# Optimization experiments

Hardware: AMD Instinct MI355X
Metric: run time of the kernel (lower is better)

Reference implementation:

```python
import jax, jax.numpy as jnp
import numpy as np
from jax.scipy.linalg import expm

D = 3  # matrix size, hard-coded by final view(a, b, 3, 3) in the torch module


def _fnn(t, W1, b1, W2, b2):
    # FNNnew: Linear(1,5) -> tanh -> Linear(5,1); t: (T,1) -> (T,)
    return (jnp.tanh(t @ W1.T + b1) @ W2.T + b2)[:, 0]


def _path_dev(Z, A1, A2):
    # Z: (bs, T, 2). Returns X (cumulative matrix products) and X^-1, each (bs, T, D, D).
    bs, T, _ = Z.shape
    A1s = A1 - A1.T
    A2s = A2 - A2.T
    M = A1s * Z[..., 0, None, None] + A2s * Z[..., 1, None, None]  # (bs,T,D,D)
    E = jax.vmap(expm)(M.reshape(-1, D, D)).reshape(bs, T, D, D)
    X0 = jnp.broadcast_to(jnp.eye(D, dtype=Z.dtype), (bs, D, D))

    def step(X, Et):
        Xn = jnp.einsum('bij,bjk->bik', X, Et)
        return Xn, Xn

    _, Xs = jax.lax.scan(step, X0, jnp.moveaxis(E[:, 1:], 0, 1))  # (T-1,bs,D,D)
    A = jnp.moveaxis(jnp.concatenate([X0[None], Xs], axis=0), 0, 1)  # (bs,T,D,D)
    B = jnp.linalg.inv(A)
    return A, B


def setup_inputs() -> dict:
    key = jax.random.key(0)
    ks = jax.random.split(key, 20)
    bs, T = 128, 4096
    inp = {"x_data": jax.random.normal(ks[0], (bs, T, 2), jnp.float32),
           "A1": jax.random.normal(ks[1], (D, D), jnp.float32),
           "A2": jax.random.normal(ks[2], (D, D), jnp.float32)}
    i = 3
    for name in ("f", "fp", "g", "gp"):
        inp[name + "_W1"] = jax.random.normal(ks[i], (5, 1), jnp.float32) * 0.5; i += 1
        inp[name + "_b1"] = jax.random.normal(ks[i], (5,), jnp.float32) * 0.5; i += 1
        inp[name + "_W2"] = jax.random.normal(ks[i], (1, 5), jnp.float32) * 0.5; i += 1
        inp[name + "_b2"] = jax.random.normal(ks[i], (1,), jnp.float32) * 0.5; i += 1
    return inp


def reference(x_data, A1, A2, f_W1, f_b1, f_W2, f_b2, fp_W1, fp_b1, fp_W2, fp_b2,
              g_W1, g_b1, g_W2, g_b2, gp_W1, gp_b1, gp_W2, gp_b2):
    bs, T, _ = x_data.shape
    t = jnp.arange(T, dtype=jnp.float32)[:, None]
    f_arr = _fnn(t, f_W1, f_b1, f_W2, f_b2)[::-1]
    fp_arr = _fnn(t, fp_W1, fp_b1, fp_W2, fp_b2)[::-1]
    g_arr = _fnn(t, g_W1, g_b1, g_W2, g_b2)
    gp_arr = _fnn(t, gp_W1, gp_b1, gp_W2, gp_b2)
    pad1 = lambda a: jnp.pad(a, (T - 1, T - 1))  # length 3T-2
    Hf = jnp.fft.fft(pad1(f_arr))
    Hfp = jnp.fft.fft(pad1(fp_arr))
    Hg = jnp.fft.fft(pad1(g_arr))
    Hgp = jnp.fft.fft(pad1(gp_arr))

    X, Xinv = _path_dev(x_data, A1, A2)
    Xf = X.reshape(bs, T, D * D)
    Xif = Xinv.reshape(bs, T, D * D)
    padT = lambda a: jnp.pad(a, ((0, 0), (T - 1, T - 1), (0, 0)))
    FA = jnp.fft.fft(padT(Xif), axis=1)  # (bs, 3T-2, 9), batched over all d^2 channels
    FB = jnp.fft.fft(padT(Xf), axis=1)
    AA = jnp.fft.ifft(FA * Hf[None, :, None], axis=1)
    AB = jnp.fft.ifft(FB * Hg[None, :, None], axis=1)
    BA = jnp.fft.ifft(FA * Hfp[None, :, None], axis=1)
    BB = jnp.fft.ifft(FB * Hgp[None, :, None], axis=1)
    out = (AA * AB + BA * BB)[:, 2 * T - 2:, :]  # (bs, T, 9)
    return out.real.reshape(bs, T, D, D)
```

## Files before the change

### kernel.cpp

```cpp
#include <hip/hip_runtime.h>
#include <math.h>

#define TT    4096
#define NFFT  8192
#define LOGN  13
#define NTHR  512
#define BS    128
#define NTASK 576
#define BUFSZ (NFFT + NFFT/8)

__device__ __forceinline__ float2 cmulf(float2 u, float2 v){
  return make_float2(u.x*v.x - u.y*v.y, u.x*v.y + u.y*v.x);
}
__device__ __forceinline__ float2 cadd(float2 a, float2 b){ return make_float2(a.x+b.x, a.y+b.y); }
__device__ __forceinline__ float2 csub(float2 a, float2 b){ return make_float2(a.x-b.x, a.y-b.y); }
__device__ __forceinline__ float2 cmuli (float2 a){ return make_float2(-a.y,  a.x); }
__device__ __forceinline__ float2 cmulni(float2 a){ return make_float2( a.y, -a.x); }

__device__ __forceinline__ float2& BREF(float2* b, int i){ return b[i + (i>>3)]; }

constexpr int ctz_c(int v){ int c=0; while(!(v&1)){ v>>=1; c++; } return c; }

template<int S>
__device__ __forceinline__ void fwd_pass(float2* buf, int tid){
  constexpr int LS = ctz_c(S);
  const float nis = -3.14159265358979f / (2.0f * (float)S);
  #pragma unroll
  for (int r = 0; r < (NFFT/4)/NTHR; ++r){
    int j   = tid + NTHR*r;
    int off = j & (S-1);
    int i0  = ((j >> LS) << (LS+2)) + off;
    float2 a = BREF(buf,i0), b = BREF(buf,i0+S), c = BREF(buf,i0+2*S), d = BREF(buf,i0+3*S);
    float sn, cs; __sincosf(nis*(float)off, &sn, &cs);
    float2 wA = make_float2(cs, sn);
    float2 wB = make_float2(cs*cs - sn*sn, 2.f*cs*sn);
    float2 w3 = cmulf(wA, wB);
    float2 s02 = cadd(a,c), d02 = csub(a,c);
    float2 s13 = cadd(b,d), d13 = csub(b,d);
    BREF(buf,i0)     = cadd(s02, s13);
    BREF(buf,i0+S)   = cmulf(csub(s02, s13), wB);
    BREF(buf,i0+2*S) = cmulf(wA, cadd(d02, cmulni(d13)));
    BREF(buf,i0+3*S) = cmulf(w3, cadd(d02, cmuli (d13)));
  }
}

template<int S>
__device__ __forceinline__ void inv_pass(float2* buf, int tid){
  constexpr int LS = ctz_c(S);
  const float pis = 3.14159265358979f / (2.0f * (float)S);
  #pragma unroll
  for (int r = 0; r < (NFFT/4)/NTHR; ++r){
    int j   = tid + NTHR*r;
    int off = j & (S-1);
    int i0  = ((j >> LS) << (LS+2)) + off;
    float2 a = BREF(buf,i0), b = BREF(buf,i0+S), c = BREF(buf,i0+2*S), d = BREF(buf,i0+3*S);
    float sn, cs; __sincosf(pis*(float)off, &sn, &cs);
    float2 u  = make_float2(cs, sn);
    float2 u2 = make_float2(cs*cs - sn*sn, 2.f*cs*sn);
    float2 u2b = cmulf(u2, b), u2d = cmulf(u2, d);
    float2 t0 = cadd(a,u2b), t1 = csub(a,u2b);
    float2 t2 = cadd(c,u2d), t3 = csub(c,u2d);
    float2 ut2  = cmulf(u, t2);
    float2 iut3 = cmuli(cmulf(u, t3));
    BREF(buf,i0)     = cadd(t0, ut2);
    BREF(buf,i0+2*S) = csub(t0, ut2);
    BREF(buf,i0+S)   = cadd(t1, iut3);
    BREF(buf,i0+3*S) = csub(t1, iut3);
  }
}

__device__ __forceinline__ void fwd_final8(float2* buf, int tid){
  const float R2 = 0.70710678118654752f;
  #pragma unroll
  for (int r = 0; r < (NFFT/8)/NTHR; ++r){
    int m = tid + NTHR*r;
    float2 v[8];
    #pragma unroll
    for (int l=0;l<8;l++) v[l] = BREF(buf,8*m+l);
    { float2 t = csub(v[0], v[4]); v[0] = cadd(v[0], v[4]); v[4] = t; }
    { float2 t = csub(v[1], v[5]); v[1] = cadd(v[1], v[5]); v[5] = cmulf(t, make_float2(R2, -R2)); }
    { float2 t = csub(v[2], v[6]); v[2] = cadd(v[2], v[6]); v[6] = cmulni(t); }
    { float2 t = csub(v[3], v[7]); v[3] = cadd(v[3], v[7]); v[7] = cmulf(t, make_float2(-R2, -R2)); }
    #pragma unroll
    for (int base = 0; base < 8; base += 4){
      { float2 t = csub(v[base],   v[base+2]); v[base]   = cadd(v[base],   v[base+2]); v[base+2] = t; }
      { float2 t = csub(v[base+1], v[base+3]); v[base+1] = cadd(v[base+1], v[base+3]); v[base+3] = cmulni(t); }
    }
    #pragma unroll
    for (int p = 0; p < 8; p += 2){ float2 t = csub(v[p], v[p+1]); v[p] = cadd(v[p], v[p+1]); v[p+1] = t; }
    #pragma unroll
    for (int l=0;l<8;l++) BREF(buf,8*m+l) = v[l];
  }
}

__device__ __forceinline__ void fwd_final8_reg(float2* buf, int tid, float2* zreg){
  const float R2 = 0.70710678118654752f;
  #pragma unroll
  for (int rr = 0; rr < 2; ++rr){
    int m = tid + NTHR*rr;
    float2 v[8];
    #pragma unroll
    for (int l=0;l<8;l++) v[l] = BREF(buf,8*m+l);
    { float2 t = csub(v[0], v[4]); v[0] = cadd(v[0], v[4]); v[4] = t; }
    { float2 t = csub(v[1], v[5]); v[1] = cadd(v[1], v[5]); v[5] = cmulf(t, make_float2(R2, -R2)); }
    { float2 t = csub(v[2], v[6]); v[2] = cadd(v[2], v[6]); v[6] = cmulni(t); }
    { float2 t = csub(v[3], v[7]); v[3] = cadd(v[3], v[7]); v[7] = cmulf(t, make_float2(-R2, -R2)); }
    #pragma unroll
    for (int base = 0; base < 8; base += 4){
      { float2 t = csub(v[base],   v[base+2]); v[base]   = cadd(v[base],   v[base+2]); v[base+2] = t; }
      { float2 t = csub(v[base+1], v[base+3]); v[base+1] = cadd(v[base+1], v[base+3]); v[base+3] = cmulni(t); }
    }
    #pragma unroll
    for (int p = 0; p < 8; p += 2){ float2 t = csub(v[p], v[p+1]); v[p] = cadd(v[p], v[p+1]); v[p+1] = t; }
    #pragma unroll
    for (int l=0;l<8;l++) zreg[rr*8+l] = v[l];
  }
}

__device__ __forceinline__ void inv_zh(float2* buf, int tid,
                                       const float2* zreg,
                                       const float2* __restrict__ H,
                                       float2* yout){
  const float R2 = 0.70710678118654752f;
  #pragma unroll
  for (int rr = 0; rr < 2; ++rr){
    int m = tid + NTHR*rr;
    float2 v[8];
    #pragma unroll
    for (int l = 0; l < 8; ++l) v[l] = cmulf(zreg[rr*8+l], H[8*m+l]);
    #pragma unroll
    for (int p = 0; p < 8; p += 2){ float2 t = v[p+1]; v[p+1] = csub(v[p], t); v[p] = cadd(v[p], t); }
    #pragma unroll
    for (int base = 0; base < 8; base += 4){
      { float2 t = v[base+2];        v[base+2] = csub(v[base],   t); v[base]   = cadd(v[base],   t); }
      { float2 t = cmuli(v[base+3]); v[base+3] = csub(v[base+1], t); v[base+1] = cadd(v[base+1], t); }
    }
    { float2 t = v[4];                              v[4] = csub(v[0], t); v[0] = cadd(v[0], t); }
    { float2 t = cmulf(v[5], make_float2(R2, R2));  v[5] = csub(v[1], t); v[1] = cadd(v[1], t); }
    { float2 t = cmuli(v[6]);                       v[6] = csub(v[2], t); v[2] = cadd(v[2], t); }
    { float2 t = cmulf(v[7], make_float2(-R2, R2)); v[7] = csub(v[3], t); v[3] = cadd(v[3], t); }
    #pragma unroll
    for (int l = 0; l < 8; ++l) BREF(buf,8*m+l) = v[l];
  }
  __syncthreads();
  inv_pass<8>(buf, tid);   __syncthreads();
  inv_pass<32>(buf, tid);  __syncthreads();
  inv_pass<128>(buf, tid); __syncthreads();
  inv_pass<512>(buf, tid); __syncthreads();
  const float pis = 3.14159265358979f / 4096.f;
  #pragma unroll
  for (int r = 0; r < 4; ++r){
    int j = tid + NTHR*r;
    float sn, cs; __sincosf(pis*(float)j, &sn, &cs);
    float2 u  = make_float2(cs, sn);
    float2 u2 = make_float2(cs*cs - sn*sn, 2.f*cs*sn);
    float2 a = BREF(buf,j), b = BREF(buf,j+2048), c = BREF(buf,j+4096), d = BREF(buf,j+6144);
    float2 u2b = cmulf(u2, b), u2d = cmulf(u2, d);
    float2 t0 = cadd(a, u2b), t1 = csub(a, u2b);
    float2 t2 = cadd(c, u2d), t3 = csub(c, u2d);
    yout[2*r]   = cadd(t0, cmulf(u, t2));
    yout[2*r+1] = cadd(t1, cmuli(cmulf(u, t3)));
  }
}

__device__ __forceinline__ void rot3(float ax, float ay, float az, float* R){
  float th2 = ax*ax + ay*ay + az*az;
  float s1, s2;
  if (th2 < 1e-8f){
    s1 = 1.f - th2*(1.f/6.f);
    s2 = 0.5f - th2*(1.f/24.f);
  } else {
    float th = sqrtf(th2);
    float sn = sinf(th);
    s1 = sn / th;
    float sh = sinf(0.5f*th);
    s2 = 2.f*sh*sh / th2;
  }
  R[0] = 1.f - s2*(ay*ay+az*az);
  R[1] = -s1*az + s2*ax*ay;
  R[2] =  s1*ay + s2*ax*az;
  R[3] =  s1*az + s2*ax*ay;
  R[4] = 1.f - s2*(ax*ax+az*az);
  R[5] = -s1*ax + s2*ay*az;
  R[6] = -s1*ay + s2*ax*az;
  R[7] =  s1*ax + s2*ay*az;
  R[8] = 1.f - s2*(ax*ax+ay*ay);
}

__device__ __forceinline__ void mm3(const float* A, const float* B, float* C){
  #pragma unroll
  for (int i=0;i<3;i++){
    float a0=A[3*i], a1=A[3*i+1], a2=A[3*i+2];
    #pragma unroll
    for (int l=0;l<3;l++)
      C[3*i+l] = a0*B[l] + a1*B[3+l] + a2*B[6+l];
  }
}

__global__ __launch_bounds__(NTHR) void prep(
  const float* __restrict__ x, const float* __restrict__ A1, const float* __restrict__ A2,
  const float* fW1, const float* fb1p, const float* fW2, const float* fb2p,
  const float* fpW1, const float* fpb1, const float* fpW2, const float* fpb2,
  const float* gW1, const float* gb1, const float* gW2, const float* gb2,
  const float* gpW1, const float* gpb1, const float* gpW2, const float* gpb2,
  float* __restrict__ X, float2* __restrict__ Hcf, float2* __restrict__ Hcf2,
  float2* __restrict__ Hcg, float2* __restrict__ Hcg2)
{
  __shared__ float2 buf[BUFSZ];
  int tid = threadIdx.x;
  if (blockIdx.x < 2){
    const float *aW1,*ab1,*aW2,*ab2,*bW1,*bb1,*bW2,*bb2; float2 *outp, *outp2; int revd;
    if (blockIdx.x == 0){ aW1=fW1; ab1=fb1p; aW2=fW2; ab2=fb2p;
      bW1=fpW1; bb1=fpb1; bW2=fpW2; bb2=fpb2; outp=Hcf; outp2=Hcf2; revd=1; }
    else { aW1=gW1; ab1=gb1; aW2=gW2; ab2=gb2;
      bW1=gpW1; bb1=gpb1; bW2=gpW2; bb2=gpb2; outp=Hcg; outp2=Hcg2; revd=0; }
    float w1a[5],b1a[5],w2a[5],w1b[5],b1b[5],w2b[5];
    #pragma unroll
    for (int h=0;h<5;h++){
      w1a[h]=aW1[h]; b1a[h]=ab1[h]; w2a[h]=aW2[h];
      w1b[h]=bW1[h]; b1b[h]=bb1[h]; w2b[h]=bW2[h];
    }
    float cA = ab2[0], cB = bb2[0];
    const float nis = -3.14159265358979f / 4096.f;
    #pragma unroll
    for (int r = 0; r < 2048/NTHR; ++r){
      int j = tid + NTHR*r;
      float2 zz[2];
      #pragma unroll
      for (int h2 = 0; h2 < 2; ++h2){
        int n = j + 2048*h2;
        float t = revd ? (float)(TT-1-n) : (float)n;
        float va = cA, vb = cB;
        #pragma unroll
        for (int h=0;h<5;h++){
          va += w2a[h]*tanhf(w1a[h]*t + b1a[h]);
          vb += w2b[h]*tanhf(w1b[h]*t + b1b[h]);
        }
        zz[h2] = make_float2(va, vb);
      }
      float sn, cs; __sincosf(nis*(float)j, &sn, &cs);
      float2 wA = make_float2(cs, sn);
      float2 wB = make_float2(cs*cs - sn*sn, 2.f*cs*sn);
      float2 w3 = cmulf(wA, wB);
      float2 a = zz[0], b = zz[1];
      BREF(buf,j)      = cadd(a,b);
      BREF(buf,j+2048) = cmulf(csub(a,b), wB);
      BREF(buf,j+4096) = cmulf(wA, make_float2(a.x + b.y, a.y - b.x));
      BREF(buf,j+6144) = cmulf(w3, make_float2(a.x - b.y, a.y + b.x));
    }
    __syncthreads(); fwd_pass<512>(buf, tid);
    __syncthreads(); fwd_pass<128>(buf, tid);
    __syncthreads(); fwd_pass<32>(buf, tid);
    __syncthreads(); fwd_pass<8>(buf, tid);
    __syncthreads(); fwd_final8(buf, tid);
    __syncthreads();
    #pragma unroll
    for (int r=0;r<NFFT/NTHR;r++){
      int p = tid + NTHR*r;
      outp[p] = BREF(buf,p);
      int k  = (int)(__brev((unsigned)p) >> (32-LOGN));
      int kk = (NFFT - k) & (NFFT-1);
      int q  = (int)(__brev((unsigned)kk) >> (32-LOGN));
      float2 z = BREF(buf,q);
      outp2[p] = make_float2(z.x, -z.y);
    }
  } else {
    float* sc = (float*)buf;
    int b = blockIdx.x - 2, j = tid;
    float k1x = A1[7]-A1[5], k1y = A1[2]-A1[6], k1z = A1[3]-A1[1];
    float k2x = A2[7]-A2[5], k2y = A2[2]-A2[6], k2z = A2[3]-A2[1];
    float L[9] = {1,0,0, 0,1,0, 0,0,1};
    #pragma unroll 1
    for (int k=1;k<=8;k++){
      int t = 8*j + k;
      if (t < TT){
        float z0 = x[((size_t)b*TT + t)*2 + 0];
        float z1 = x[((size_t)b*TT + t)*2 + 1];
        float R[9];
        rot3(k1x*z0 + k2x*z1, k1y*z0 + k2y*z1, k1z*z0 + k2z*z1, R);
        float Cm[9]; mm3(L, R, Cm);
        #pragma unroll
        for (int m=0;m<9;m++) L[m] = Cm[m];
      }
    }
    #pragma unroll
    for (int m=0;m<9;m++) sc[(0*512 + j)*9 + m] = L[m];
    int cur = 0;
    for (int d=1; d<512; d<<=1){
      __syncthreads();
      float own[9], res[9];
      #pragma unroll
      for (int m=0;m<9;m++) own[m] = sc[(cur*512 + j)*9 + m];
      if (j >= d){
        float prev[9];
        #pragma unroll
        for (int m=0;m<9;m++) prev[m] = sc[(cur*512 + j - d)*9 + m];
        mm3(prev, own, res);
      } else {
        #pragma unroll
        for (int m=0;m<9;m++) res[m] = own[m];
      }
      #pragma unroll
      for (int m=0;m<9;m++) sc[((cur^1)*512 + j)*9 + m] = res[m];
      cur ^= 1;
    }
    __syncthreads();
    float Xc[9];
    if (j == 0){
      Xc[0]=1;Xc[1]=0;Xc[2]=0;Xc[3]=0;Xc[4]=1;Xc[5]=0;Xc[6]=0;Xc[7]=0;Xc[8]=1;
    } else {
      #pragma unroll
      for (int m=0;m<9;m++) Xc[m] = sc[(cur*512 + j - 1)*9 + m];
    }
    #pragma unroll
    for (int m=0;m<9;m++) X[((size_t)b*9 + m)*TT + 8*j] = Xc[m];
    #pragma unroll 1
    for (int k=1;k<8;k++){
      int t = 8*j + k;
      float z0 = x[((size_t)b*TT + t)*2 + 0];
      float z1 = x[((size_t)b*TT + t)*2 + 1];
      float R[9];
      rot3(k1x*z0 + k2x*z1, k1y*z0 + k2y*z1, k1z*z0 + k2z*z1, R);
      float Cm[9]; mm3(Xc, R, Cm);
      #pragma unroll
      for (int m=0;m<9;m++){ Xc[m] = Cm[m]; X[((size_t)b*9 + m)*TT + t] = Xc[m]; }
    }
  }
}

__global__ __launch_bounds__(NTHR, 2) void convk4(const float* __restrict__ X,
    const float2* __restrict__ Hcf, const float2* __restrict__ Hcf2,
    const float2* __restrict__ Hcg, const float2* __restrict__ Hcg2,
    float* __restrict__ tmp)
{
  __shared__ float2 buf[BUFSZ];
  int tid = threadIdx.x;
  int task = blockIdx.x;
  int b1i, c1, b2i, c2; bool cross;
  if (task < 384){
    int b = task/3, p = task % 3;
    b1i = b; b2i = b; cross = true;
    c1 = (p==0)?1:((p==1)?2:5);
    c2 = (p==0)?3:((p==1)?6:7);
  } else if (task < 512){
    int b = task - 384; b1i=b; b2i=b; c1=0; c2=4; cross=false;
  } else {
    int q = task - 512; b1i = 2*q; b2i = 2*q+1; c1=8; c2=8; cross=false;
  }
  const float* x1 = X + ((size_t)b1i*9 + c1)*TT;
  const float* x2 = X + ((size_t)b2i*9 + c2)*TT;

  {
    const float nis = -3.14159265358979f / 4096.f;
    #pragma unroll
    for (int r = 0; r < 2048/NTHR; ++r){
      int j = tid + NTHR*r;
      float2 a = make_float2(x1[j], x2[j]);
      float2 b = make_float2(x1[j+2048], x2[j+2048]);
      float sn, cs; __sincosf(nis*(float)j, &sn, &cs);
      float2 wA = make_float2(cs, sn);
      float2 wB = make_float2(cs*cs - sn*sn, 2.f*cs*sn);
      float2 w3 = cmulf(wA, wB);
      BREF(buf,j)      = cadd(a,b);
      BREF(buf,j+2048) = cmulf(csub(a,b), wB);
      BREF(buf,j+4096) = cmulf(wA, make_float2(a.x + b.y, a.y - b.x));
      BREF(buf,j+6144) = cmulf(w3, make_float2(a.x - b.y, a.y + b.x));
    }
  }
  __syncthreads(); fwd_pass<512>(buf, tid);
  __syncthreads(); fwd_pass<128>(buf, tid);
  __syncthreads(); fwd_pass<32>(buf, tid);
  __syncthreads(); fwd_pass<8>(buf, tid);
  __syncthreads();
  float2 zreg[16];
  fwd_final8_reg(buf, tid, zreg);

  float2 W1[8];
  inv_zh(buf, tid, zreg, Hcf, W1);
  __syncthreads();
  float2 W2[8];
  inv_zh(buf, tid, zreg, Hcf2, W2);
  float a1[8], a2[8], bb1[8], bb2[8];
  #pragma unroll
  for (int e = 0; e < 8; ++e){
    a1[e]  = 0.5f*(W1[e].x + W2[e].x);
    a2[e]  = 0.5f*(W1[e].y + W2[e].y);
    bb1[e] = 0.5f*(W1[e].y - W2[e].y);
    bb2[e] = 0.5f*(W2[e].x - W1[e].x);
  }
  __syncthreads();
  float2 V1[8];
  inv_zh(buf, tid, zreg, Hcg, V1);
  __syncthreads();
  float2 V2[8];
  inv_zh(buf, tid, zreg, Hcg2, V2);

  const float invN2 = (1.0f/NFFT)*(1.0f/NFFT);
  float* op1 = tmp + ((size_t)b1i*9 + c1)*TT;
  float* op2 = tmp + ((size_t)b2i*9 + c2)*TT;
  #pragma unroll
  for (int r = 0; r < 4; ++r){
    #pragma unroll
    for (int h = 0; h < 2; ++h){
      int e = 2*r + h;
      int s = tid + NTHR*r + h*2048;
      float c1v = 0.5f*(V1[e].x + V2[e].x);
      float c2v = 0.5f*(V1[e].y + V2[e].y);
      float d1  = 0.5f*(V1[e].y - V2[e].y);
      float d2  = 0.5f*(V2[e].x - V1[e].x);
      float Af1 = cross ? a2[e]  : a1[e];
      float Bf1 = cross ? bb2[e] : bb1[e];
      float Af2 = cross ? a1[e]  : a2[e];
      float Bf2 = cross ? bb1[e] : bb2[e];
      op1[s] = (Af1*c1v + Bf1*d1) * invN2;
      op2[s] = (Af2*c2v + Bf2*d2) * invN2;
    }
  }
}

__global__ __launch_bounds__(256) void repack(const float* __restrict__ tmp,
                                              float* __restrict__ out){
  __shared__ float tile[9][264];
  int b  = blockIdx.x >> 4;
  int t0 = (blockIdx.x & 15) << 8;
  int tid = threadIdx.x;
  #pragma unroll
  for (int c = 0; c < 9; ++c)
    tile[c][tid] = tmp[((size_t)b*9 + c)*TT + t0 + tid];
  __syncthreads();
  size_t base = ((size_t)b*TT + t0)*9;
  #pragma unroll
  for (int k = 0; k < 9; ++k){
    int idx = tid + 256*k;
    out[base + idx] = tile[idx % 9][idx / 9];
  }
}

__device__ void fft_dif_bitrev(float2* buf, int tid){
  const float PI = 3.14159265358979f;
  #pragma unroll 1
  for (int stage = 0; stage < LOGN; ++stage){
    int logspan = LOGN - 1 - stage;
    int span = 1 << logspan;
    float nis = -PI / (float)span;
    __syncthreads();
    #pragma unroll
    for (int r = 0; r < NFFT/2/NTHR; ++r){
      int j = tid + NTHR*r;
      int off = j & (span - 1);
      int i0 = ((j >> logspan) << (logspan + 1)) + off;
      int i1 = i0 + span;
      float2 a = buf[i0], b = buf[i1];
      float ang = nis * (float)off;
      float sn, cs;
      __sincosf(ang, &sn, &cs);
      float2 d = make_float2(a.x - b.x, a.y - b.y);
      buf[i0] = make_float2(a.x + b.x, a.y + b.y);
      buf[i1] = cmulf(d, make_float2(cs, sn));
    }
  }
  __syncthreads();
  #pragma unroll
  for (int r = 0; r < NFFT/NTHR; ++r){
    int p = tid + NTHR*r;
    int q = (int)(__brev((unsigned)p) >> (32 - LOGN));
    if (p < q){ float2 t = buf[p]; buf[p] = buf[q]; buf[q] = t; }
  }
  __syncthreads();
}

__global__ __launch_bounds__(NTHR) void hker_fb(
  const float* fW1, const float* fb1p, const float* fW2, const float* fb2p,
  const float* fpW1, const float* fpb1, const float* fpW2, const float* fpb2,
  const float* gW1, const float* gb1, const float* gW2, const float* gb2,
  const float* gpW1, const float* gpb1, const float* gpW2, const float* gpb2,
  float2* Hcf, float2* Hcg)
{
  __shared__ float2 buf[NFFT];
  int tid = threadIdx.x;
  const float *aW1,*ab1,*aW2,*ab2,*bW1,*bb1,*bW2,*bb2; float2* outp; int revd;
  if (blockIdx.x == 0){ aW1=fW1; ab1=fb1p; aW2=fW2; ab2=fb2p;
    bW1=fpW1; bb1=fpb1; bW2=fpW2; bb2=fpb2; outp=Hcf; revd=1; }
  else { aW1=gW1; ab1=gb1; aW2=gW2; ab2=gb2;
    bW1=gpW1; bb1=gpb1; bW2=gpW2; bb2=gpb2; outp=Hcg; revd=0; }
  float w1a[5],b1a[5],w2a[5],w1b[5],b1b[5],w2b[5];
  #pragma unroll
  for (int h=0;h<5;h++){
    w1a[h]=aW1[h]; b1a[h]=ab1[h]; w2a[h]=aW2[h];
    w1b[h]=bW1[h]; b1b[h]=bb1[h]; w2b[h]=bW2[h];
  }
  float cA = ab2[0], cB = bb2[0];
  for (int r=0;r<NFFT/NTHR;r++){
    int s = tid + NTHR*r;
    float2 v = make_float2(0.f, 0.f);
    if (s < TT){
      float t = revd ? (float)(TT-1-s) : (float)s;
      float va = cA, vb = cB;
      #pragma unroll
      for (int h=0;h<5;h++){
        va += w2a[h]*tanhf(w1a[h]*t + b1a[h]);
        vb += w2b[h]*tanhf(w1b[h]*t + b1b[h]);
      }
      v = make_float2(va, vb);
    }
    buf[s] = v;
  }
  fft_dif_bitrev(buf, tid);
  for (int r=0;r<NFFT/NTHR;r++){ int k = tid + NTHR*r; outp[k] = buf[k]; }
}

__global__ __launch_bounds__(256) void scank_fb(const float* __restrict__ x,
    const float* __restrict__ A1, const float* __restrict__ A2,
    float* __restrict__ X)
{
  __shared__ float sc[2][256][9];
  int b = blockIdx.x, j = threadIdx.x;
  float k1x = A1[7]-A1[5], k1y = A1[2]-A1[6], k1z = A1[3]-A1[1];
  float k2x = A2[7]-A2[5], k2y = A2[2]-A2[6], k2z = A2[3]-A2[1];
  float L[9] = {1,0,0, 0,1,0, 0,0,1};
  #pragma unroll 1
  for (int k=1;k<=16;k++){
    int t = 16*j + k;
    if (t < TT){
      float z0 = x[((size_t)b*TT + t)*2 + 0];
      float z1 = x[((size_t)b*TT + t)*2 + 1];
      float R[9];
      rot3(k1x*z0 + k2x*z1, k1y*z0 + k2y*z1, k1z*z0 + k2z*z1, R);
      float Cm[9]; mm3(L, R, Cm);
      #pragma unroll
      for (int m=0;m<9;m++) L[m] = Cm[m];
    }
  }
  #pragma unroll
  for (int m=0;m<9;m++) sc[0][j][m] = L[m];
  int cur = 0;
  for (int d=1; d<256; d<<=1){
    __syncthreads();
    float own[9], res[9];
    #pragma unroll
    for (int m=0;m<9;m++) own[m] = sc[cur][j][m];
    if (j >= d){
      float prev[9];
      #pragma unroll
      for (int m=0;m<9;m++) prev[m] = sc[cur][j-d][m];
      mm3(prev, own, res);
    } else {
      #pragma unroll
      for (int m=0;m<9;m++) res[m] = own[m];
    }
    #pragma unroll
    for (int m=0;m<9;m++) sc[cur^1][j][m] = res[m];
    cur ^= 1;
  }
  __syncthreads();
  float Xc[9];
  if (j == 0){
    Xc[0]=1;Xc[1]=0;Xc[2]=0;Xc[3]=0;Xc[4]=1;Xc[5]=0;Xc[6]=0;Xc[7]=0;Xc[8]=1;
  } else {
    #pragma unroll
    for (int m=0;m<9;m++) Xc[m] = sc[cur][j-1][m];
  }
  #pragma unroll
  for (int m=0;m<9;m++) X[((size_t)b*9 + m)*TT + 16*j] = Xc[m];
  #pragma unroll 1
  for (int k=1;k<16;k++){
    int t = 16*j + k;
    float z0 = x[((size_t)b*TT + t)*2 + 0];
    float z1 = x[((size_t)b*TT + t)*2 + 1];
    float R[9];
    rot3(k1x*z0 + k2x*z1, k1y*z0 + k2y*z1, k1z*z0 + k2z*z1, R);
    float Cm[9]; mm3(Xc, R, Cm);
    #pragma unroll
    for (int m=0;m<9;m++){ Xc[m] = Cm[m]; X[((size_t)b*9 + m)*TT + t] = Xc[m]; }
  }
}

__global__ __launch_bounds__(NTHR) void convk_fb(const float* __restrict__ X,
    const float2* __restrict__ Hcf, const float2* __restrict__ Hcg,
    float* __restrict__ out)
{
  __shared__ float2 buf[NFFT];
  __shared__ float2 fb1[NFFT/2 + 2];
  __shared__ float2 fb2[NFFT/2 + 2];
  int tid = threadIdx.x;
  int task = blockIdx.x;
  int b1i, c1, b2i, c2; bool cross;
  if (task < 384){
    int b = task/3, p = task % 3;
    b1i = b; b2i = b; cross = true;
    c1 = (p==0)?1:((p==1)?2:5);
    c2 = (p==0)?3:((p==1)?6:7);
  } else if (task < 512){
    int b = task - 384; b1i=b; b2i=b; c1=0; c2=4; cross=false;
  } else {
    int q = task - 512; b1i = 2*q; b2i = 2*q+1; c1=8; c2=8; cross=false;
  }
  const float* x1 = X + ((size_t)b1i*9 + c1)*TT;
  const float* x2 = X + ((size_t)b2i*9 + c2)*TT;
  #pragma unroll
  for (int r=0;r<NFFT/NTHR;r++){
    int s = tid + NTHR*r;
    float2 v = make_float2(0.f,0.f);
    if (s < TT){ v.x = x1[s]; v.y = x2[s]; }
    buf[s] = v;
  }
  fft_dif_bitrev(buf, tid);
  for (int k = tid; k <= NFFT/2; k += NTHR){
    int kk = (NFFT - k) & (NFFT - 1);
    float2 zk = buf[k], zn = buf[kk];
    fb1[k] = make_float2(0.5f*(zk.x + zn.x), 0.5f*(zk.y - zn.y));
    fb2[k] = make_float2(0.5f*(zk.y + zn.y), 0.5f*(zn.x - zk.x));
  }
  __syncthreads();
  const float invN2 = (1.0f/NFFT)*(1.0f/NFFT);
  #pragma unroll 1
  for (int pass = 0; pass < 2; ++pass){
    const float2* fA = (pass==0) ? (cross ? fb2 : fb1) : (cross ? fb1 : fb2);
    const float2* fG = (pass==0) ? fb1 : fb2;
    int ob = (pass==0) ? b1i : b2i;
    int oc = (pass==0) ? c1 : c2;
    #pragma unroll
    for (int r=0;r<NFFT/NTHR;r++){
      int k = tid + NTHR*r;
      float2 F;
      if (k <= NFFT/2) F = fA[k];
      else { float2 g = fA[NFFT-k]; F = make_float2(g.x, -g.y); }
      float2 P = cmulf(F, Hcf[k]);
      buf[k] = make_float2(P.x, -P.y);
    }
    fft_dif_bitrev(buf, tid);
    float rA[8], rB[8];
    #pragma unroll
    for (int r=0;r<8;r++){
      int s = tid + NTHR*r;
      rA[r] = buf[s].x;
      rB[r] = -buf[s].y;
    }
    #pragma unroll
    for (int r=0;r<NFFT/NTHR;r++){
      int k = tid + NTHR*r;
      float2 F;
      if (k <= NFFT/2) F = fG[k];
      else { float2 g = fG[NFFT-k]; F = make_float2(g.x, -g.y); }
      float2 P = cmulf(F, Hcg[k]);
      buf[k] = make_float2(P.x, -P.y);
    }
    fft_dif_bitrev(buf, tid);
    #pragma unroll
    for (int r=0;r<8;r++){
      int s = tid + NTHR*r;
      float AB = buf[s].x, BB = -buf[s].y;
      out[((size_t)ob*TT + s)*9 + oc] = (rA[r]*AB + rB[r]*BB) * invN2;
    }
  }
}

extern "C" void kernel_launch(void* const* d_in, const int* in_sizes, int n_in,
                              void* d_out, int out_size, void* d_ws, size_t ws_size,
                              hipStream_t stream){
  const float* x  = (const float*)d_in[0];
  const float* A1 = (const float*)d_in[1];
  const float* A2 = (const float*)d_in[2];
  const float* P[16];
  for (int i=0;i<16;i++) P[i] = (const float*)d_in[3+i];

  size_t xbytes = (size_t)BS*9*TT*sizeof(float);
  size_t hbytes = (size_t)NFFT*sizeof(float2);
  float*  Xb   = (float*)d_ws;
  float2* Hcf  = (float2*)((char*)d_ws + xbytes);
  float2* Hcf2 = Hcf + NFFT;
  float2* Hcg  = Hcf + 2*NFFT;
  float2* Hcg2 = Hcf + 3*NFFT;
  float*  tmp  = (float*)((char*)d_ws + xbytes + 4*hbytes);
  size_t need = xbytes + 4*hbytes + xbytes;

  if (ws_size >= need){
    prep<<<2 + BS, NTHR, 0, stream>>>(x, A1, A2,
        P[0],P[1],P[2],P[3],P[4],P[5],P[6],P[7],
        P[8],P[9],P[10],P[11],P[12],P[13],P[14],P[15],
        Xb, Hcf, Hcf2, Hcg, Hcg2);
    convk4<<<NTASK, NTHR, 0, stream>>>(Xb, Hcf, Hcf2, Hcg, Hcg2, tmp);
    repack<<<BS*16, 256, 0, stream>>>(tmp, (float*)d_out);
  } else {
    hker_fb<<<2, NTHR, 0, stream>>>(P[0],P[1],P[2],P[3],P[4],P[5],P[6],P[7],
        P[8],P[9],P[10],P[11],P[12],P[13],P[14],P[15], Hcf, Hcg);
    scank_fb<<<BS, 256, 0, stream>>>(x, A1, A2, Xb);
    convk_fb<<<NTASK, NTHR, 0, stream>>>(Xb, Hcf, Hcg, (float*)d_out);
  }
}
```

Before: 215.6 us.

## Restructure shared-memory FFTs as radix-16 register passes with XOR-swizzled LDS

Replaces the radix-4 shared-memory FFT passes (five forward passes plus a radix-8 final, and likewise for each inverse) with radix-16 butterflies computed in registers. Each 8192-point transform now takes about three shared-memory round trips instead of six, with a final radix-2 step folded in. The padded BREF indexing is replaced by an XOR swizzle to avoid bank conflicts, which also shrinks the LDS buffer. This cuts barrier count and LDS traffic, but the 16-element register arrays raise register pressure, which could cost occupancy. The H multiply layout must also match the new ordering.

After: 273.5 us. 26.9% more time.

```diff
diff --git a/kernel.cpp b/kernel.cpp
--- a/kernel.cpp
+++ b/kernel.cpp
@@ -16,10 +16,167 @@
 __device__ __forceinline__ float2 csub(float2 a, float2 b){ return make_float2(a.x-b.x, a.y-b.y); }
 __device__ __forceinline__ float2 cmuli (float2 a){ return make_float2(-a.y,  a.x); }
 __device__ __forceinline__ float2 cmulni(float2 a){ return make_float2( a.y, -a.x); }
+__device__ __forceinline__ float2 csq(float2 a){ return make_float2(a.x*a.x - a.y*a.y, 2.f*a.x*a.y); }
 
 __device__ __forceinline__ float2& BREF(float2* b, int i){ return b[i + (i>>3)]; }
+#define SWZ(p) ((p) ^ (((p)>>4)&15))
+
+#define DEF_C8  const float2 C8[8]  = { {1.f,0.f},{0.9238795325f,-0.3826834324f},{0.7071067812f,-0.7071067812f},{0.3826834324f,-0.9238795325f},{0.f,-1.f},{-0.3826834324f,-0.9238795325f},{-0.7071067812f,-0.7071067812f},{-0.9238795325f,-0.3826834324f} }
+#define DEF_CC8 const float2 CC8[8] = { {1.f,0.f},{0.9238795325f, 0.3826834324f},{0.7071067812f, 0.7071067812f},{0.3826834324f, 0.9238795325f},{0.f, 1.f},{-0.3826834324f, 0.9238795325f},{-0.7071067812f, 0.7071067812f},{-0.9238795325f, 0.3826834324f} }
 
 constexpr int ctz_c(int v){ int c=0; while(!(v&1)){ v>>=1; c++; } return c; }
+
+__device__ __forceinline__ void rad16_fwd_tail(float2* v, float2 u2){
+  DEF_C8;
+  float2 u3 = csq(u2), u4 = csq(u3);
+  #pragma unroll
+  for (int g=0; g<16; g+=8)
+    #pragma unroll
+    for (int t=0;t<4;t++){
+      float2 a=v[g+t], b=v[g+t+4];
+      v[g+t]=cadd(a,b);
+      v[g+t+4]=cmulf(csub(a,b), cmulf(u2, C8[2*t]));
+    }
+  #pragma unroll
+  for (int g=0; g<16; g+=4)
+    #pragma unroll
+    for (int t=0;t<2;t++){
+      float2 a=v[g+t], b=v[g+t+2];
+      v[g+t]=cadd(a,b);
+      v[g+t+2]=cmulf(csub(a,b), cmulf(u3, C8[4*t]));
+    }
+  #pragma unroll
+  for (int g=0; g<16; g+=2){
+    float2 a=v[g], b=v[g+1];
+    v[g]=cadd(a,b);
+    v[g+1]=cmulf(csub(a,b), u4);
+  }
+}
+
+__device__ __forceinline__ void rad16_fwd(float2* v, float2 u1){
+  DEF_C8;
+  #pragma unroll
+  for (int t=0;t<8;t++){
+    float2 a=v[t], b=v[t+8];
+    v[t]=cadd(a,b);
+    v[t+8]=cmulf(csub(a,b), cmulf(u1, C8[t]));
+  }
+  rad16_fwd_tail(v, csq(u1));
+}
+
+__device__ __forceinline__ void rad16_inv(float2* v, float2 u1c){
+  DEF_CC8;
+  float2 u2c = csq(u1c), u3c = csq(u2c), u4c = csq(u3c);
+  #pragma unroll
+  for (int g=0; g<16; g+=2){
+    float2 b = cmulf(v[g+1], u4c);
+    float2 a = v[g];
+    v[g]=cadd(a,b); v[g+1]=csub(a,b);
+  }
+  #pragma unroll
+  for (int g=0; g<16; g+=4)
+    #pragma unroll
+    for (int t=0;t<2;t++){
+      float2 b = cmulf(v[g+t+2], cmulf(u3c, CC8[4*t]));
+      float2 a = v[g+t];
+      v[g+t]=cadd(a,b); v[g+t+2]=csub(a,b);
+    }
+  #pragma unroll
+  for (int g=0; g<16; g+=8)
+    #pragma unroll
+    for (int t=0;t<4;t++){
+      float2 b = cmulf(v[g+t+4], cmulf(u2c, CC8[2*t]));
+      float2 a = v[g+t];
+      v[g+t]=cadd(a,b); v[g+t+4]=csub(a,b);
+    }
+  #pragma unroll
+  for (int t=0;t<8;t++){
+    float2 b = cmulf(v[t+8], cmulf(u1c, CC8[t]));
+    float2 a = v[t];
+    v[t]=cadd(a,b); v[t+8]=csub(a,b);
+  }
+}
+
+__device__ __forceinline__ void rad16_inv_last(float2* v, float2 u1c, float2* y){
+  DEF_CC8;
+  float2 u2c = csq(u1c), u3c = csq(u2c), u4c = csq(u3c);
+  #pragma unroll
+  for (int g=0; g<16; g+=2){
+    float2 b = cmulf(v[g+1], u4c);
+    float2 a = v[g];
+    v[g]=cadd(a,b); v[g+1]=csub(a,b);
+  }
+  #pragma unroll
+  for (int g=0; g<16; g+=4)
+    #pragma unroll
+    for (int t=0;t<2;t++){
+      float2 b = cmulf(v[g+t+2], cmulf(u3c, CC8[4*t]));
+      float2 a = v[g+t];
+      v[g+t]=cadd(a,b); v[g+t+2]=csub(a,b);
+    }
+  #pragma unroll
+  for (int g=0; g<16; g+=8)
+    #pragma unroll
+    for (int t=0;t<4;t++){
+      float2 b = cmulf(v[g+t+4], cmulf(u2c, CC8[2*t]));
+      float2 a = v[g+t];
+      v[g+t]=cadd(a,b); v[g+t+4]=csub(a,b);
+    }
+  #pragma unroll
+  for (int t=0;t<8;t++)
+    y[t] = cadd(v[t], cmulf(v[t+8], cmulf(u1c, CC8[t])));
+}
+
+template<bool FIRST>
+__device__ __forceinline__ void inv16(float2* buf, int tid,
+                                      const float2* zreg,
+                                      const float2* __restrict__ H,
+                                      float2* y){
+  if (!FIRST) __syncthreads();
+  {
+    float2 v[16];
+    const float2* Hp = H + 16*tid;
+    #pragma unroll
+    for (int j=0;j<16;j++) v[j] = cmulf(zreg[j], Hp[j]);
+    #pragma unroll
+    for (int g=0; g<16; g+=2){
+      float2 a=v[g], b=v[g+1];
+      v[g]=cadd(a,b); v[g+1]=csub(a,b);
+    }
+    #pragma unroll
+    for (int j=0;j<16;j++) buf[SWZ(16*tid + j)] = v[j];
+  }
+  __syncthreads();
+  {
+    float2 v[16];
+    int base = 32*(tid>>1), c = tid&1;
+    #pragma unroll
+    for (int t=0;t<16;t++) v[t] = buf[SWZ(base + c + 2*t)];
+    float2 u1c = c ? make_float2(0.9807852804f, 0.1950903220f) : make_float2(1.f, 0.f);
+    rad16_inv(v, u1c);
+    #pragma unroll
+    for (int t=0;t<16;t++) buf[SWZ(base + c + 2*t)] = v[t];
+  }
+  __syncthreads();
+  {
+    float2 v[16];
+    int base = 512*(tid>>5), c = tid&31;
+    #pragma unroll
+    for (int t=0;t<16;t++) v[t] = buf[SWZ(base + c + 32*t)];
+    float sn, cs; __sincosf(3.14159265358979f*(float)c/256.f, &sn, &cs);
+    rad16_inv(v, make_float2(cs, sn));
+    #pragma unroll
+    for (int t=0;t<16;t++) buf[SWZ(base + c + 32*t)] = v[t];
+  }
+  __syncthreads();
+  {
+    float2 v[16];
+    #pragma unroll
+    for (int t=0;t<16;t++) v[t] = buf[SWZ(tid + 512*t)];
+    float sn, cs; __sincosf(3.14159265358979f*(float)tid/4096.f, &sn, &cs);
+    rad16_inv_last(v, make_float2(cs, sn), y);
+  }
+}
 
 template<int S>
 __device__ __forceinline__ void fwd_pass(float2* buf, int tid){
@@ -44,31 +201,6 @@
   }
 }
 
-template<int S>
-__device__ __forceinline__ void inv_pass(float2* buf, int tid){
-  constexpr int LS = ctz_c(S);
-  const float pis = 3.14159265358979f / (2.0f * (float)S);
-  #pragma unroll
-  for (int r = 0; r < (NFFT/4)/NTHR; ++r){
-    int j   = tid + NTHR*r;
-    int off = j & (S-1);
-    int i0  = ((j >> LS) << (LS+2)) + off;
-    float2 a = BREF(buf,i0), b = BREF(buf,i0+S), c = BREF(buf,i0+2*S), d = BREF(buf,i0+3*S);
-    float sn, cs; __sincosf(pis*(float)off, &sn, &cs);
-    float2 u  = make_float2(cs, sn);
-    float2 u2 = make_float2(cs*cs - sn*sn, 2.f*cs*sn);
-    float2 u2b = cmulf(u2, b), u2d = cmulf(u2, d);
-    float2 t0 = cadd(a,u2b), t1 = csub(a,u2b);
-    float2 t2 = cadd(c,u2d), t3 = csub(c,u2d);
-    float2 ut2  = cmulf(u, t2);
-    float2 iut3 = cmuli(cmulf(u, t3));
-    BREF(buf,i0)     = cadd(t0, ut2);
-    BREF(buf,i0+2*S) = csub(t0, ut2);
-    BREF(buf,i0+S)   = cadd(t1, iut3);
-    BREF(buf,i0+3*S) = csub(t1, iut3);
-  }
-}
-
 __device__ __forceinline__ void fwd_final8(float2* buf, int tid){
   const float R2 = 0.70710678118654752f;
   #pragma unroll
@@ -90,76 +222,6 @@
     for (int p = 0; p < 8; p += 2){ float2 t = csub(v[p], v[p+1]); v[p] = cadd(v[p], v[p+1]); v[p+1] = t; }
     #pragma unroll
     for (int l=0;l<8;l++) BREF(buf,8*m+l) = v[l];
-  }
-}
-
-__device__ __forceinline__ void fwd_final8_reg(float2* buf, int tid, float2* zreg){
-  const float R2 = 0.70710678118654752f;
-  #pragma unroll
-  for (int rr = 0; rr < 2; ++rr){
-    int m = tid + NTHR*rr;
-    float2 v[8];
-    #pragma unroll
-    for (int l=0;l<8;l++) v[l] = BREF(buf,8*m+l);
-    { float2 t = csub(v[0], v[4]); v[0] = cadd(v[0], v[4]); v[4] = t; }
-    { float2 t = csub(v[1], v[5]); v[1] = cadd(v[1], v[5]); v[5] = cmulf(t, make_float2(R2, -R2)); }
-    { float2 t = csub(v[2], v[6]); v[2] = cadd(v[2], v[6]); v[6] = cmulni(t); }
-    { float2 t = csub(v[3], v[7]); v[3] = cadd(v[3], v[7]); v[7] = cmulf(t, make_float2(-R2, -R2)); }
-    #pragma unroll
-    for (int base = 0; base < 8; base += 4){
-      { float2 t = csub(v[base],   v[base+2]); v[base]   = cadd(v[base],   v[base+2]); v[base+2] = t; }
-      { float2 t = csub(v[base+1], v[base+3]); v[base+1] = cadd(v[base+1], v[base+3]); v[base+3] = cmulni(t); }
-    }
-    #pragma unroll
-    for (int p = 0; p < 8; p += 2){ float2 t = csub(v[p], v[p+1]); v[p] = cadd(v[p], v[p+1]); v[p+1] = t; }
-    #pragma unroll
-    for (int l=0;l<8;l++) zreg[rr*8+l] = v[l];
-  }
-}
-
-__device__ __forceinline__ void inv_zh(float2* buf, int tid,
-                                       const float2* zreg,
-                                       const float2* __restrict__ H,
-                                       float2* yout){
-  const float R2 = 0.70710678118654752f;
-  #pragma unroll
-  for (int rr = 0; rr < 2; ++rr){
-    int m = tid + NTHR*rr;
-    float2 v[8];
-    #pragma unroll
-    for (int l = 0; l < 8; ++l) v[l] = cmulf(zreg[rr*8+l], H[8*m+l]);
-    #pragma unroll
-    for (int p = 0; p < 8; p += 2){ float2 t = v[p+1]; v[p+1] = csub(v[p], t); v[p] = cadd(v[p], t); }
-    #pragma unroll
-    for (int base = 0; base < 8; base += 4){
-      { float2 t = v[base+2];        v[base+2] = csub(v[base],   t); v[base]   = cadd(v[base],   t); }
-      { float2 t = cmuli(v[base+3]); v[base+3] = csub(v[base+1], t); v[base+1] = cadd(v[base+1], t); }
-    }
-    { float2 t = v[4];                              v[4] = csub(v[0], t); v[0] = cadd(v[0], t); }
-    { float2 t = cmulf(v[5], make_float2(R2, R2));  v[5] = csub(v[1], t); v[1] = cadd(v[1], t); }
-    { float2 t = cmuli(v[6]);                       v[6] = csub(v[2], t); v[2] = cadd(v[2], t); }
-    { float2 t = cmulf(v[7], make_float2(-R2, R2)); v[7] = csub(v[3], t); v[3] = cadd(v[3], t); }
-    #pragma unroll
-    for (int l = 0; l < 8; ++l) BREF(buf,8*m+l) = v[l];
-  }
-  __syncthreads();
-  inv_pass<8>(buf, tid);   __syncthreads();
-  inv_pass<32>(buf, tid);  __syncthreads();
-  inv_pass<128>(buf, tid); __syncthreads();
-  inv_pass<512>(buf, tid); __syncthreads();
-  const float pis = 3.14159265358979f / 4096.f;
-  #pragma unroll
-  for (int r = 0; r < 4; ++r){
-    int j = tid + NTHR*r;
-    float sn, cs; __sincosf(pis*(float)j, &sn, &cs);
-    float2 u  = make_float2(cs, sn);
-    float2 u2 = make_float2(cs*cs - sn*sn, 2.f*cs*sn);
-    float2 a = BREF(buf,j), b = BREF(buf,j+2048), c = BREF(buf,j+4096), d = BREF(buf,j+6144);
-    float2 u2b = cmulf(u2, b), u2d = cmulf(u2, d);
-    float2 t0 = cadd(a, u2b), t1 = csub(a, u2b);
-    float2 t2 = cadd(c, u2d), t3 = csub(c, u2d);
-    yout[2*r]   = cadd(t0, cmulf(u, t2));
-    yout[2*r+1] = cadd(t1, cmuli(cmulf(u, t3)));
   }
 }
 
@@ -328,12 +390,12 @@
   }
 }
 
-__global__ __launch_bounds__(NTHR, 2) void convk4(const float* __restrict__ X,
+__global__ __launch_bounds__(NTHR, 2) void convk5(const float* __restrict__ X,
     const float2* __restrict__ Hcf, const float2* __restrict__ Hcf2,
     const float2* __restrict__ Hcg, const float2* __restrict__ Hcg2,
     float* __restrict__ tmp)
 {
-  __shared__ float2 buf[BUFSZ];
+  __shared__ float2 buf[NFFT];
   int tid = threadIdx.x;
   int task = blockIdx.x;
   int b1i, c1, b2i, c2; bool cross;
@@ -351,70 +413,86 @@
   const float* x2 = X + ((size_t)b2i*9 + c2)*TT;
 
   {
-    const float nis = -3.14159265358979f / 4096.f;
-    #pragma unroll
-    for (int r = 0; r < 2048/NTHR; ++r){
-      int j = tid + NTHR*r;
-      float2 a = make_float2(x1[j], x2[j]);
-      float2 b = make_float2(x1[j+2048], x2[j+2048]);
-      float sn, cs; __sincosf(nis*(float)j, &sn, &cs);
-      float2 wA = make_float2(cs, sn);
-      float2 wB = make_float2(cs*cs - sn*sn, 2.f*cs*sn);
-      float2 w3 = cmulf(wA, wB);
-      BREF(buf,j)      = cadd(a,b);
-      BREF(buf,j+2048) = cmulf(csub(a,b), wB);
-      BREF(buf,j+4096) = cmulf(wA, make_float2(a.x + b.y, a.y - b.x));
-      BREF(buf,j+6144) = cmulf(w3, make_float2(a.x - b.y, a.y + b.x));
-    }
-  }
-  __syncthreads(); fwd_pass<512>(buf, tid);
-  __syncthreads(); fwd_pass<128>(buf, tid);
-  __syncthreads(); fwd_pass<32>(buf, tid);
-  __syncthreads(); fwd_pass<8>(buf, tid);
+    float2 v[16];
+    DEF_C8;
+    #pragma unroll
+    for (int t=0;t<8;t++){
+      int n = tid + 512*t;
+      v[t] = make_float2(x1[n], x2[n]);
+    }
+    float sn, cs; __sincosf(-3.14159265358979f*(float)tid/4096.f, &sn, &cs);
+    float2 u1 = make_float2(cs, sn);
+    #pragma unroll
+    for (int t=0;t<8;t++) v[t+8] = cmulf(v[t], cmulf(u1, C8[t]));
+    rad16_fwd_tail(v, csq(u1));
+    #pragma unroll
+    for (int t=0;t<16;t++) buf[SWZ(tid + 512*t)] = v[t];
+  }
+  __syncthreads();
+  {
+    float2 v[16];
+    int base = 512*(tid>>5), c = tid&31;
+    #pragma unroll
+    for (int t=0;t<16;t++) v[t] = buf[SWZ(base + c + 32*t)];
+    float sn, cs; __sincosf(-3.14159265358979f*(float)c/256.f, &sn, &cs);
+    rad16_fwd(v, make_float2(cs, sn));
+    #pragma unroll
+    for (int t=0;t<16;t++) buf[SWZ(base + c + 32*t)] = v[t];
+  }
+  __syncthreads();
+  {
+    float2 v[16];
+    int base = 32*(tid>>1), c = tid&1;
+    #pragma unroll
+    for (int t=0;t<16;t++) v[t] = buf[SWZ(base + c + 2*t)];
+    float2 u1 = c ? make_float2(0.9807852804f, -0.1950903220f) : make_float2(1.f, 0.f);
+    rad16_fwd(v, u1);
+    #pragma unroll
+    for (int t=0;t<16;t++) buf[SWZ(base + c + 2*t)] = v[t];
+  }
   __syncthreads();
   float2 zreg[16];
-  fwd_final8_reg(buf, tid, zreg);
-
-  float2 W1[8];
-  inv_zh(buf, tid, zreg, Hcf, W1);
-  __syncthreads();
-  float2 W2[8];
-  inv_zh(buf, tid, zreg, Hcf2, W2);
+  {
+    #pragma unroll
+    for (int j=0;j<16;j++) zreg[j] = buf[SWZ(16*tid + j)];
+    #pragma unroll
+    for (int g=0; g<16; g+=2){
+      float2 a = zreg[g], b = zreg[g+1];
+      zreg[g] = cadd(a,b); zreg[g+1] = csub(a,b);
+    }
+  }
+
+  float2 w1y[8], w2y[8];
+  inv16<true >(buf, tid, zreg, Hcf,  w1y);
+  inv16<false>(buf, tid, zreg, Hcf2, w2y);
   float a1[8], a2[8], bb1[8], bb2[8];
   #pragma unroll
   for (int e = 0; e < 8; ++e){
-    a1[e]  = 0.5f*(W1[e].x + W2[e].x);
-    a2[e]  = 0.5f*(W1[e].y + W2[e].y);
-    bb1[e] = 0.5f*(W1[e].y - W2[e].y);
-    bb2[e] = 0.5f*(W2[e].x - W1[e].x);
-  }
-  __syncthreads();
-  float2 V1[8];
-  inv_zh(buf, tid, zreg, Hcg, V1);
-  __syncthreads();
-  float2 V2[8];
-  inv_zh(buf, tid, zreg, Hcg2, V2);
+    a1[e]  = 0.5f*(w1y[e].x + w2y[e].x);
+    a2[e]  = 0.5f*(w1y[e].y + w2y[e].y);
+    bb1[e] = 0.5f*(w1y[e].y - w2y[e].y);
+    bb2[e] = 0.5f*(w2y[e].x - w1y[e].x);
+  }
+  float2 v1y[8], v2y[8];
+  inv16<false>(buf, tid, zreg, Hcg,  v1y);
+  inv16<false>(buf, tid, zreg, Hcg2, v2y);
 
   const float invN2 = (1.0f/NFFT)*(1.0f/NFFT);
   float* op1 = tmp + ((size_t)b1i*9 + c1)*TT;
   float* op2 = tmp + ((size_t)b2i*9 + c2)*TT;
   #pragma unroll
-  for (int r = 0; r < 4; ++r){
-    #pragma unroll
-    for (int h = 0; h < 2; ++h){
-      int e = 2*r + h;
-      int s = tid + NTHR*r + h*2048;
-      float c1v = 0.5f*(V1[e].x + V2[e].x);
-      float c2v = 0.5f*(V1[e].y + V2[e].y);
-      float d1  = 0.5f*(V1[e].y - V2[e].y);
-      float d2  = 0.5f*(V2[e].x - V1[e].x);
-      float Af1 = cross ? a2[e]  : a1[e];
-      float Bf1 = cross ? bb2[e] : bb1[e];
-      float Af2 = cross ? a1[e]  : a2[e];
-      float Bf2 = cross ? bb1[e] : bb2[e];
-      op1[s] = (Af1*c1v + Bf1*d1) * invN2;
-      op2[s] = (Af2*c2v + Bf2*d2) * invN2;
-    }
+  for (int e = 0; e < 8; ++e){
+    int s = tid + 512*e;
+    float c1v = 0.5f*(v1y[e].x + v2y[e].x);
+    float c2v = 0.5f*(v1y[e].y + v2y[e].y);
+    float d1  = 0.5f*(v1y[e].y - v2y[e].y);
+    float d2  = 0.5f*(v2y[e].x - v1y[e].x);
+    float Af1 = cross ? a2[e]  : a1[e];
+    float Bf1 = cross ? bb2[e] : bb1[e];
+    float Af2 = cross ? a1[e]  : a2[e];
+    float Bf2 = cross ? bb1[e] : bb2[e];
+    op1[s] = (Af1*c1v + Bf1*d1) * invN2;
+    op2[s] = (Af2*c2v + Bf2*d2) * invN2;
   }
 }
 
@@ -679,7 +757,7 @@
         P[0],P[1],P[2],P[3],P[4],P[5],P[6],P[7],
         P[8],P[9],P[10],P[11],P[12],P[13],P[14],P[15],
         Xb, Hcf, Hcf2, Hcg, Hcg2);
-    convk4<<<NTASK, NTHR, 0, stream>>>(Xb, Hcf, Hcf2, Hcg, Hcg2, tmp);
+    convk5<<<NTASK, NTHR, 0, stream>>>(Xb, Hcf, Hcf2, Hcg, Hcg2, tmp);
     repack<<<BS*16, 256, 0, stream>>>(tmp, (float*)d_out);
   } else {
     hker_fb<<<2, NTHR, 0, stream>>>(P[0],P[1],P[2],P[3],P[4],P[5],P[6],P[7],
```
